# Kernel optimization log

Hardware: AMD Instinct MI355X
Metric: run time of the kernel (lower is better)

## Reference

```python
import jax, jax.numpy as jnp
import numpy as np

K = 3
PAD = 1
DIL = 1
BN_EPS = 1e-5


def _unfold(x, k, pad, dil):
    # torch F.unfold with stride=1: (bs, c, h, w) -> (bs, c*k*k, h*w), c slowest.
    bs, c, h, w = x.shape
    xp = jnp.pad(x, ((0, 0), (0, 0), (pad, pad), (pad, pad)))
    cols = [xp[:, :, i * dil:i * dil + h, j * dil:j * dil + w]
            for i in range(k) for j in range(k)]
    return jnp.stack(cols, axis=2).reshape(bs, c * k * k, h * w)


def setup_inputs() -> dict:
    key = jax.random.key(0)
    ks = jax.random.split(key, 4)
    bs, c, h, w = 8, 3, 512, 512
    kk = K * K
    kernel = jax.random.normal(ks[0], (bs, kk, h, w), jnp.float32)
    inp = jax.random.normal(ks[1], (bs, c, h, w), jnp.float32)
    inp0 = jax.random.normal(ks[2], (bs, c, h, w), jnp.float32)
    conv_w = jax.random.normal(ks[3], (kk, kk * 3, 3, 3), jnp.float32) * 0.05
    return {
        "kernel": kernel,
        "input": inp,
        "input0": inp0,
        "conv_w": conv_w,
        "bn_gamma": jnp.ones((kk,), jnp.float32),
        "bn_beta": jnp.zeros((kk,), jnp.float32),
        "bn_mean": jnp.zeros((kk,), jnp.float32),
        "bn_var": jnp.ones((kk,), jnp.float32),
    }


def reference(kernel, input, input0, conv_w, bn_gamma, bn_beta, bn_mean, bn_var):
    bs, c, h, w = input.shape
    kk = K * K
    mid = (kk - 1) // 2  # 4 for K=3
    # im2col: (bs, c*k*k, h*w) = (bs, 27, hw)
    im = _unfold(input, K, PAD, DIL)
    # overwrite 3 center rows with input0
    im = im.at[:, mid:mid + 3, :].set(input0.reshape(bs, c, h * w))
    x = im.reshape(bs, c * kk, h, w)
    # 3x3 conv, 27 -> 9 channels, pad 1, no bias
    y = jax.lax.conv_general_dilated(
        x, conv_w, window_strides=(1, 1), padding=[(1, 1), (1, 1)],
        dimension_numbers=("NCHW", "OIHW", "NCHW"))
    # BatchNorm (inference: running stats)
    scale = (bn_gamma / jnp.sqrt(bn_var + BN_EPS))[None, :, None, None]
    shift = (bn_beta - bn_mean * bn_gamma / jnp.sqrt(bn_var + BN_EPS))[None, :, None, None]
    y = y * scale + shift
    # elementwise weighted reduce over the k*k axis
    out = jnp.einsum("bkp,bkp->bp", y.reshape(bs, kk, h * w),
                     kernel.reshape(bs, kk, h * w))
    return out.reshape(bs, 1, h, w)
```

## Files before the change

### kernel.cpp

```cpp
#include <hip/hip_runtime.h>

#define HW 512
#define CH 3
#define KK 9
#define BS 8
#define TW 64
#define TH 16


__global__ __launch_bounds__(256) void prep_kernel(
    const float* __restrict__ conv_w, const float* __restrict__ gamma,
    const float* __restrict__ beta, const float* __restrict__ mean,
    const float* __restrict__ var, float* __restrict__ ws) {
  const int tid = threadIdx.x;
  for (int t = tid; t < 675; t += 256) {
    int o = t % 9, tap = t / 9;
    int c = tap / 25, r = tap % 25, ey = r / 5, ex = r % 5;
    float s = gamma[o] * rsqrtf(var[o] + 1e-5f);
    float sum = 0.f;
    for (int dy = 0; dy < 3; ++dy) {
      int oy = ey - dy; if (oy < 0 || oy > 2) continue;
      for (int dx = 0; dx < 3; ++dx) {
        int ox = ex - dx; if (ox < 0 || ox > 2) continue;
        int off = oy * 3 + ox;
        if (c == 0 && off >= 4 && off <= 6) continue;
        sum += conv_w[((o * 27 + c * 9 + off) * 3 + dy) * 3 + dx];
      }
    }
    ws[(c * 5 + ey) * 48 + ex * 9 + o] = s * sum;
  }
  for (int t = tid; t < 243; t += 256) {
    int o = t % 9, tap = t / 9;
    int c = tap / 9, r = tap % 9;
    float s = gamma[o] * rsqrtf(var[o] + 1e-5f);
    int ey = r / 3, ex = r % 3;
    ws[720 + c * 96 + r * 9 + o] =
        s * conv_w[((o * 27 + 4 + c) * 3 + ey) * 3 + ex];
  }
  for (int o = tid; o < 9; o += 256) {
    float s = gamma[o] * rsqrtf(var[o] + 1e-5f);
    ws[1008 + o] = beta[o] - mean[o] * s;
  }
  for (int t = tid; t < 2187; t += 256) {
    int o = t % 9, q = t / 9;
    int ic = q / 9, r = q % 9, dy = r / 3, dx = r % 3;
    float s = gamma[o] * rsqrtf(var[o] + 1e-5f);
    ws[1024 + t] = s * conv_w[((o * 27 + ic) * 3 + dy) * 3 + dx];
  }
}

__global__ __launch_bounds__(256) void main_kernel(
    const float* __restrict__ kern, const float* __restrict__ input,
    const float* __restrict__ input0, const float* __restrict__ ws,
    float* __restrict__ out) {
  __shared__ __align__(16) float in_t[3][TH + 4][TW + 4];
  __shared__ __align__(16) float in0_t[3][TH + 2][TW + 4];
  const int tid = threadIdx.x;
  const int b = blockIdx.z;
  const int x0 = blockIdx.x * TW, y0 = blockIdx.y * TH;
  const float* inp_b = input + (long)b * CH * HW * HW;
  const float* inp0_b = input0 + (long)b * CH * HW * HW;

  float* lin = &in_t[0][0][0];
  for (int i = tid; i < 3 * (TH + 4) * (TW + 4); i += 256) {
    int c = i / ((TH + 4) * (TW + 4));
    int r = i % ((TH + 4) * (TW + 4));
    int ry = r / (TW + 4), rx = r % (TW + 4);
    int gy = y0 + ry - 2, gx = x0 + rx - 2;
    float v = 0.f;
    if ((unsigned)gy < HW && (unsigned)gx < HW) v = inp_b[(c * HW + gy) * HW + gx];
    lin[i] = v;
  }
  float* lin0 = &in0_t[0][0][0];
  for (int i = tid; i < 3 * (TH + 2) * (TW + 4); i += 256) {
    int c = i / ((TH + 2) * (TW + 4));
    int r = i % ((TH + 2) * (TW + 4));
    int ry = r / (TW + 4), rx = r % (TW + 4);
    int gy = y0 + ry - 1, gx = x0 + rx - 1;
    float v = 0.f;
    if ((unsigned)gy < HW && (unsigned)gx < HW) v = inp0_b[(c * HW + gy) * HW + gx];
    lin0[i] = v;
  }
  __syncthreads();

  const int tx = tid & 15, ty = tid >> 4;
  const int bx = tx * 4;
  const int Y = y0 + ty;

  float acc[9][4];
#pragma unroll
  for (int o = 0; o < 9; ++o)
#pragma unroll
    for (int p = 0; p < 4; ++p) acc[o][p] = 0.f;

#pragma unroll 1
  for (int c = 0; c < 3; ++c) {
#pragma unroll 1
    for (int ey = 0; ey < 5; ++ey) {
      const float4 lo = *(const float4*)(&in_t[c][ty + ey][bx]);
      const float4 hi = *(const float4*)(&in_t[c][ty + ey][bx + 4]);
      const float win[8] = {lo.x, lo.y, lo.z, lo.w, hi.x, hi.y, hi.z, hi.w};
      const float* wg = ws + (c * 5 + ey) * 48;
#pragma unroll
      for (int ex = 0; ex < 5; ++ex)
#pragma unroll
        for (int o = 0; o < 9; ++o) {
          const float w = wg[ex * 9 + o];
#pragma unroll
          for (int p = 0; p < 4; ++p)
            acc[o][p] = fmaf(w, win[ex + p], acc[o][p]);
        }
    }
  }

#pragma unroll 1
  for (int c = 0; c < 3; ++c) {
#pragma unroll 1
    for (int ey = 0; ey < 3; ++ey) {
      const float4 lo = *(const float4*)(&in0_t[c][ty + ey][bx]);
      const float4 hi = *(const float4*)(&in0_t[c][ty + ey][bx + 4]);
      const float win[8] = {lo.x, lo.y, lo.z, lo.w, hi.x, hi.y, hi.z, hi.w};
      const float* wg = ws + 720 + c * 96 + ey * 27;
#pragma unroll
      for (int ex = 0; ex < 3; ++ex)
#pragma unroll
        for (int o = 0; o < 9; ++o) {
          const float w = wg[ex * 9 + o];
#pragma unroll
          for (int p = 0; p < 4; ++p)
            acc[o][p] = fmaf(w, win[ex + p], acc[o][p]);
        }
    }
  }

  const long hw2 = (long)HW * HW;
  const float* kb = kern + (long)b * KK * hw2 + (long)Y * HW + (x0 + bx);
  float res0 = 0.f, res1 = 0.f, res2 = 0.f, res3 = 0.f;
#pragma unroll
  for (int o = 0; o < 9; ++o) {
    const float sh = ws[1008 + o];
    const float4 k4 = *(const float4*)(kb + (long)o * hw2);
    res0 = fmaf(k4.x, acc[o][0] + sh, res0);
    res1 = fmaf(k4.y, acc[o][1] + sh, res1);
    res2 = fmaf(k4.z, acc[o][2] + sh, res2);
    res3 = fmaf(k4.w, acc[o][3] + sh, res3);
  }
  *(float4*)(out + ((long)b * HW + Y) * HW + (x0 + bx)) =
      make_float4(res0, res1, res2, res3);
}

__global__ __launch_bounds__(256) void border_kernel(
    const float* __restrict__ kern, const float* __restrict__ input,
    const float* __restrict__ input0, const float* __restrict__ ws,
    float* __restrict__ out) {
  const int per_img = 4 * HW - 4;
  int idx = blockIdx.x * blockDim.x + threadIdx.x;
  if (idx >= BS * per_img) return;
  int b = idx / per_img, p = idx % per_img;
  int X, Y;
  if (p < HW) { Y = 0; X = p; }
  else if (p < 2 * HW) { Y = HW - 1; X = p - HW; }
  else if (p < 3 * HW - 2) { X = 0; Y = p - 2 * HW + 1; }
  else { X = HW - 1; Y = p - (3 * HW - 2) + 1; }

  const float* inp_b = input + (long)b * CH * HW * HW;
  const float* inp0_b = input0 + (long)b * CH * HW * HW;
  float acc[9];
#pragma unroll
  for (int o = 0; o < 9; ++o) acc[o] = 0.f;

  for (int dy = 0; dy < 3; ++dy) {
    int yy = Y + dy - 1;
    if ((unsigned)yy >= HW) continue;
    for (int dx = 0; dx < 3; ++dx) {
      int xx = X + dx - 1;
      if ((unsigned)xx >= HW) continue;
      for (int c = 0; c < 3; ++c)
        for (int oy = 0; oy < 3; ++oy) {
          int iy = yy + oy - 1;
          for (int ox = 0; ox < 3; ++ox) {
            int off = oy * 3 + ox;
            if (c == 0 && off >= 4 && off <= 6) continue;
            int ix = xx + ox - 1;
            float v = 0.f;
            if ((unsigned)iy < HW && (unsigned)ix < HW)
              v = inp_b[(c * HW + iy) * HW + ix];
            const float* w = ws + 1024 + ((c * 9 + off) * 9 + dy * 3 + dx) * 9;
#pragma unroll
            for (int o = 0; o < 9; ++o) acc[o] = fmaf(w[o], v, acc[o]);
          }
        }
      for (int c = 0; c < 3; ++c) {
        float v = inp0_b[(c * HW + yy) * HW + xx];
        const float* w = ws + 720 + c * 96 + (dy * 3 + dx) * 9;
#pragma unroll
        for (int o = 0; o < 9; ++o) acc[o] = fmaf(w[o], v, acc[o]);
      }
    }
  }
  const float* kb = kern + (long)b * KK * (HW * HW) + Y * HW + X;
  float result = 0.f;
#pragma unroll
  for (int o = 0; o < 9; ++o)
    result = fmaf(kb[(long)o * (HW * HW)], acc[o] + ws[1008 + o], result);
  out[((long)b * HW + Y) * HW + X] = result;
}

extern "C" void kernel_launch(void* const* d_in, const int* in_sizes, int n_in,
                              void* d_out, int out_size, void* d_ws, size_t ws_size,
                              hipStream_t stream) {
  const float* kern   = (const float*)d_in[0];
  const float* input  = (const float*)d_in[1];
  const float* input0 = (const float*)d_in[2];
  const float* conv_w = (const float*)d_in[3];
  const float* gamma  = (const float*)d_in[4];
  const float* beta   = (const float*)d_in[5];
  const float* mean   = (const float*)d_in[6];
  const float* var    = (const float*)d_in[7];
  float* out = (float*)d_out;
  float* ws  = (float*)d_ws;

  hipLaunchKernelGGL(prep_kernel, dim3(1), dim3(256), 0, stream,
                     conv_w, gamma, beta, mean, var, ws);
  dim3 grid(HW / TW, HW / TH, BS);
  hipLaunchKernelGGL(main_kernel, grid, dim3(256), 0, stream,
                     kern, input, input0, ws, out);
  int nb = (BS * (4 * HW - 4) + 255) / 256;
  hipLaunchKernelGGL(border_kernel, dim3(nb), dim3(256), 0, stream,
                     kern, input, input0, ws, out);
}
```

Before: 241.7 us.

## Rotate shared-memory tile chunks to avoid LDS bank conflicts and fully unroll loops

Stores the input tiles in LDS as float4 chunks whose column index is rotated by the row index (mod 17), so threads in different rows reading the same column chunk hit different banks. The inner compute loops over channels and rows are fully unrolled instead of kept rolled. The aim is to cut LDS bank conflicts on the 128-bit reads and to remove loop overhead, at the cost of extra index arithmetic in both the load and compute phases and larger code and register use from unrolling.

```diff
diff --git a/kernel.cpp b/kernel.cpp
--- a/kernel.cpp
+++ b/kernel.cpp
@@ -53,39 +53,43 @@
     const float* __restrict__ kern, const float* __restrict__ input,
     const float* __restrict__ input0, const float* __restrict__ ws,
     float* __restrict__ out) {
-  __shared__ __align__(16) float in_t[3][TH + 4][TW + 4];
-  __shared__ __align__(16) float in0_t[3][TH + 2][TW + 4];
+  __shared__ float4 in_t4[3][TH + 4][17];
+  __shared__ float4 in0_t4[3][TH + 2][17];
   const int tid = threadIdx.x;
   const int b = blockIdx.z;
   const int x0 = blockIdx.x * TW, y0 = blockIdx.y * TH;
   const float* inp_b = input + (long)b * CH * HW * HW;
   const float* inp0_b = input0 + (long)b * CH * HW * HW;
 
-  float* lin = &in_t[0][0][0];
   for (int i = tid; i < 3 * (TH + 4) * (TW + 4); i += 256) {
     int c = i / ((TH + 4) * (TW + 4));
-    int r = i % ((TH + 4) * (TW + 4));
-    int ry = r / (TW + 4), rx = r % (TW + 4);
-    int gy = y0 + ry - 2, gx = x0 + rx - 2;
+    int rr = i % ((TH + 4) * (TW + 4));
+    int r = rr / (TW + 4), col = rr % (TW + 4);
+    int gy = y0 + r - 2, gx = x0 + col - 2;
     float v = 0.f;
     if ((unsigned)gy < HW && (unsigned)gx < HW) v = inp_b[(c * HW + gy) * HW + gx];
-    lin[i] = v;
-  }
-  float* lin0 = &in0_t[0][0][0];
+    int ch = (col >> 2) + r;
+    if (ch >= 17) ch -= 17;
+    if (ch >= 17) ch -= 17;
+    ((float*)&in_t4[c][r][ch])[col & 3] = v;
+  }
   for (int i = tid; i < 3 * (TH + 2) * (TW + 4); i += 256) {
     int c = i / ((TH + 2) * (TW + 4));
-    int r = i % ((TH + 2) * (TW + 4));
-    int ry = r / (TW + 4), rx = r % (TW + 4);
-    int gy = y0 + ry - 1, gx = x0 + rx - 1;
+    int rr = i % ((TH + 2) * (TW + 4));
+    int r = rr / (TW + 4), col = rr % (TW + 4);
+    int gy = y0 + r - 1, gx = x0 + col - 1;
     float v = 0.f;
     if ((unsigned)gy < HW && (unsigned)gx < HW) v = inp0_b[(c * HW + gy) * HW + gx];
-    lin0[i] = v;
+    int ch = (col >> 2) + r;
+    if (ch >= 17) ch -= 17;
+    if (ch >= 17) ch -= 17;
+    ((float*)&in0_t4[c][r][ch])[col & 3] = v;
   }
   __syncthreads();
 
   const int tx = tid & 15, ty = tid >> 4;
+  const int Y = y0 + ty;
   const int bx = tx * 4;
-  const int Y = y0 + ty;
 
   float acc[9][4];
 #pragma unroll
@@ -93,12 +97,18 @@
 #pragma unroll
     for (int p = 0; p < 4; ++p) acc[o][p] = 0.f;
 
-#pragma unroll 1
+#pragma unroll
   for (int c = 0; c < 3; ++c) {
-#pragma unroll 1
+#pragma unroll
     for (int ey = 0; ey < 5; ++ey) {
-      const float4 lo = *(const float4*)(&in_t[c][ty + ey][bx]);
-      const float4 hi = *(const float4*)(&in_t[c][ty + ey][bx + 4]);
+      const int row = ty + ey;
+      int u = tx + row;
+      if (u >= 17) u -= 17;
+      if (u >= 17) u -= 17;
+      int u2 = u + 1;
+      if (u2 >= 17) u2 -= 17;
+      const float4 lo = in_t4[c][row][u];
+      const float4 hi = in_t4[c][row][u2];
       const float win[8] = {lo.x, lo.y, lo.z, lo.w, hi.x, hi.y, hi.z, hi.w};
       const float* wg = ws + (c * 5 + ey) * 48;
 #pragma unroll
@@ -113,12 +123,18 @@
     }
   }
 
-#pragma unroll 1
+#pragma unroll
   for (int c = 0; c < 3; ++c) {
-#pragma unroll 1
+#pragma unroll
     for (int ey = 0; ey < 3; ++ey) {
-      const float4 lo = *(const float4*)(&in0_t[c][ty + ey][bx]);
-      const float4 hi = *(const float4*)(&in0_t[c][ty + ey][bx + 4]);
+      const int row = ty + ey;
+      int u = tx + row;
+      if (u >= 17) u -= 17;
+      if (u >= 17) u -= 17;
+      int u2 = u + 1;
+      if (u2 >= 17) u2 -= 17;
+      const float4 lo = in0_t4[c][row][u];
+      const float4 hi = in0_t4[c][row][u2];
       const float win[8] = {lo.x, lo.y, lo.z, lo.w, hi.x, hi.y, hi.z, hi.w};
       const float* wg = ws + 720 + c * 96 + ey * 27;
 #pragma unroll
```

Measured after the change: 251.8 us. 4.2% more time.
